# Optimization experiments

Hardware: AMD Instinct MI355X
Metric: run time of the kernel (lower is better)

The kernel has to match this reference:

```python
import jax, jax.numpy as jnp
import numpy as np

N, E, DIN, HID, DOUT = 50000, 800000, 128, 128, 64
NEG_SLOPE = 0.2


def setup_inputs() -> dict:
    key = jax.random.key(0)
    ks = jax.random.split(key, 16)
    x = jax.random.normal(ks[0], (N, DIN), dtype=jnp.float32)
    edge_index = jax.random.randint(ks[1], (2, E), 0, N, dtype=jnp.int64)

    def lin(k, fan_in, fan_out):
        kw, kb = jax.random.split(k)
        s = 1.0 / np.sqrt(fan_in)
        W = jax.random.uniform(kw, (fan_in, fan_out), jnp.float32, -s, s)
        b = jax.random.uniform(kb, (fan_out,), jnp.float32, -s, s)
        return W, b

    Wl, bl = lin(ks[2], DIN, DIN)   # GATv2 lin_l
    Wr, br = lin(ks[3], DIN, DIN)   # GATv2 lin_r
    att = jax.random.uniform(ks[4], (DIN,), jnp.float32, -1.0 / np.sqrt(DIN), 1.0 / np.sqrt(DIN))
    bg = jnp.zeros((DIN,), jnp.float32)  # GAT output bias
    W1, b1 = lin(ks[5], DIN, HID)   # ChebConv K=1 -> plain linear
    W2, b2 = lin(ks[6], HID, HID)
    W3, b3 = lin(ks[7], HID, DOUT)
    return {"x": x, "edge_index": edge_index, "Wl": Wl, "bl": bl, "Wr": Wr,
            "br": br, "att": att, "bg": bg, "W1": W1, "b1": b1,
            "W2": W2, "b2": b2, "W3": W3, "b3": b3}


def reference(x, edge_index, Wl, bl, Wr, br, att, bg, W1, b1, W2, b2, W3, b3):
    n = x.shape[0]
    # GATv2Conv adds self loops by default
    loop = jnp.arange(n, dtype=edge_index.dtype)
    src = jnp.concatenate([edge_index[0], loop])  # source j
    dst = jnp.concatenate([edge_index[1], loop])  # target i

    xl = x @ Wl + bl  # [N, DIN]
    xr = x @ Wr + br  # [N, DIN]

    # GATv2 edge scores: leaky_relu(x_l[j] + x_r[i]) . att
    e = jax.nn.leaky_relu(xl[src] + xr[dst], NEG_SLOPE)  # [E+N, DIN]
    a = e @ att                                          # [E+N]

    # softmax over incoming edges of each destination node
    amax = jax.ops.segment_max(a, dst, num_segments=n)
    ea = jnp.exp(a - amax[dst])
    denom = jax.ops.segment_sum(ea, dst, num_segments=n)
    alpha = ea / denom[dst]                              # [E+N]

    # aggregate messages alpha * x_l[j] at destinations
    h = jax.ops.segment_sum(alpha[:, None] * xl[src], dst, num_segments=n) + bg

    # ChebConv with K=1 reduces to a linear layer (T_0(L) = I)
    h = jax.nn.relu(h @ W1 + b1)
    h = jax.nn.relu(h @ W2 + b2)
    # dropout_rate = 0.0 -> identity
    return h @ W3 + b3
```

## Files before the change

### kernel.cpp

```cpp
#include <hip/hip_runtime.h>
#include <hip/hip_bf16.h>

#define DIN 128
#define NEG_SLOPE 0.2f
#define PTILE 2048
#define FCAP 8192

typedef __attribute__((ext_vector_type(8))) short bf16x8;
typedef __attribute__((ext_vector_type(8))) unsigned short u16x8;
typedef __attribute__((ext_vector_type(4))) float f32x4;

__device__ __forceinline__ ushort f2bf(float f) {
  unsigned u = __float_as_uint(f);
  u += 0x7FFFu + ((u >> 16) & 1u);
  return (ushort)(u >> 16);
}
__device__ __forceinline__ float bf2f(ushort u) {
  return __uint_as_float((unsigned)u << 16);
}

__global__ __launch_bounds__(256) void cvt_weights_kernel(
    const float* __restrict__ Wl, const float* __restrict__ Wr,
    const float* __restrict__ W1, const float* __restrict__ W2,
    const float* __restrict__ W3,
    ushort* __restrict__ WlT, ushort* __restrict__ WrT,
    ushort* __restrict__ W1T, ushort* __restrict__ W2T,
    ushort* __restrict__ W3T, int* __restrict__ ghist) {
  int i = blockIdx.x * 256 + threadIdx.x;
  if (i < 16384) {
    int k = i >> 7, c = i & 127; WlT[c * 128 + k] = f2bf(Wl[i]);
  } else if (i < 32768) {
    int j = i - 16384; int k = j >> 7, c = j & 127; WrT[c * 128 + k] = f2bf(Wr[j]);
  } else if (i < 49152) {
    int j = i - 32768; int k = j >> 7, c = j & 127; W1T[c * 128 + k] = f2bf(W1[j]);
  } else if (i < 65536) {
    int j = i - 49152; int k = j >> 7, c = j & 127; W2T[c * 128 + k] = f2bf(W2[j]);
  } else if (i < 73728) {
    int j = i - 65536; int k = j >> 6, c = j & 63; W3T[c * 128 + k] = f2bf(W3[j]);
  } else if (i < 73984) {
    ghist[i - 73728] = 0;
  }
}

__global__ __launch_bounds__(256) void lin_lr_mfma_kernel(
    const float* __restrict__ x,
    const ushort* __restrict__ WlT, const float* __restrict__ bl,
    const ushort* __restrict__ WrT, const float* __restrict__ br,
    ushort* __restrict__ xl, ushort* __restrict__ xr, int n) {
  const int tid = threadIdx.x;
  const int wv = tid >> 6, lane = tid & 63;
  const int m = lane & 15, quad = lane >> 4;
  const int colbase = (wv & 1) * 64;
  const int nodew = blockIdx.x * 32 + (wv >> 1) * 16;
  int arow = nodew + m; if (arow >= n) arow = n - 1;
  f32x4 accl[4], accr[4];
#pragma unroll
  for (int nt = 0; nt < 4; nt++) { accl[nt] = (f32x4){0,0,0,0}; accr[nt] = (f32x4){0,0,0,0}; }
#pragma unroll
  for (int kk = 0; kk < 4; kk++) {
    int k0 = kk * 32 + quad * 8;
    const float4* xp = (const float4*)(x + (long)arow * 128 + k0);
    float4 x0 = xp[0], x1 = xp[1];
    bf16x8 af;
    af[0] = (short)f2bf(x0.x); af[1] = (short)f2bf(x0.y);
    af[2] = (short)f2bf(x0.z); af[3] = (short)f2bf(x0.w);
    af[4] = (short)f2bf(x1.x); af[5] = (short)f2bf(x1.y);
    af[6] = (short)f2bf(x1.z); af[7] = (short)f2bf(x1.w);
#pragma unroll
    for (int nt = 0; nt < 4; nt++) {
      int brow = colbase + nt * 16 + m;
      bf16x8 bl8 = *(const bf16x8*)(WlT + brow * 128 + k0);
      bf16x8 br8 = *(const bf16x8*)(WrT + brow * 128 + k0);
      accl[nt] = __builtin_amdgcn_mfma_f32_16x16x32_bf16(af, bl8, accl[nt], 0, 0, 0);
      accr[nt] = __builtin_amdgcn_mfma_f32_16x16x32_bf16(af, br8, accr[nt], 0, 0, 0);
    }
  }
#pragma unroll
  for (int nt = 0; nt < 4; nt++) {
    int col = colbase + nt * 16 + m;
    float vbl = bl[col], vbr = br[col];
#pragma unroll
    for (int r = 0; r < 4; r++) {
      int node = nodew + quad * 4 + r;
      if (node < n) {
        xl[(long)node * 128 + col] = f2bf(accl[nt][r] + vbl);
        xr[(long)node * 128 + col] = f2bf(accr[nt][r] + vbr);
      }
    }
  }
}

__global__ __launch_bounds__(256) void hist_kernel(
    const int* __restrict__ ei, int* __restrict__ ghist, int E) {
  __shared__ int h[256];
  h[threadIdx.x] = 0;
  __syncthreads();
  for (int e = blockIdx.x * PTILE + threadIdx.x;
       e < min(E, (int)(blockIdx.x + 1) * PTILE); e += 256)
    atomicAdd(&h[ei[E + e] >> 8], 1);
  __syncthreads();
  if (h[threadIdx.x] > 0) atomicAdd(&ghist[threadIdx.x], h[threadIdx.x]);
}

__global__ __launch_bounds__(256) void scan_small_kernel(
    const int* __restrict__ ghist, int* __restrict__ cum,
    int* __restrict__ cursor) {
  __shared__ int sh[256];
  int tid = threadIdx.x;
  int v = ghist[tid];
  sh[tid] = v;
  __syncthreads();
  for (int d = 1; d < 256; d <<= 1) {
    int t = (tid >= d) ? sh[tid - d] : 0;
    __syncthreads();
    sh[tid] += t;
    __syncthreads();
  }
  int exc = sh[tid] - v;
  cum[tid] = exc;
  cursor[tid] = exc;
  if (tid == 255) cum[256] = sh[255];
}

__global__ __launch_bounds__(256) void partition_kernel(
    const int* __restrict__ ei, unsigned* __restrict__ part,
    int* __restrict__ cursor, int E) {
  __shared__ int hist[256], pref[256], sexcl[256], curs[256], gbase[256];
  __shared__ unsigned buf[PTILE];
  const int tid = threadIdx.x;
  const int tile0 = blockIdx.x * PTILE;
  const int tcount = min(PTILE, E - tile0);
  hist[tid] = 0;
  __syncthreads();
  unsigned pk[PTILE / 256];
  int cnt = 0;
  for (int i = tid; i < tcount; i += 256) {
    int e = tile0 + i;
    int s = ei[e], d = ei[E + e];
    unsigned p = ((unsigned)d << 16) | (unsigned)s;
    pk[cnt++] = p;
    atomicAdd(&hist[d >> 8], 1);
  }
  __syncthreads();
  int v = hist[tid];
  pref[tid] = v;
  __syncthreads();
  for (int d = 1; d < 256; d <<= 1) {
    int t = (tid >= d) ? pref[tid - d] : 0;
    __syncthreads();
    pref[tid] += t;
    __syncthreads();
  }
  int exc = pref[tid] - v;
  sexcl[tid] = exc;
  curs[tid] = exc;
  gbase[tid] = (v > 0) ? atomicAdd(&cursor[tid], v) : 0;
  __syncthreads();
  for (int j = 0; j < cnt; j++) {
    int b = pk[j] >> 24;
    int pos = atomicAdd(&curs[b], 1);
    buf[pos] = pk[j];
  }
  __syncthreads();
  for (int i = tid; i < tcount; i += 256) {
    unsigned p = buf[i];
    int b = p >> 24;
    part[gbase[b] + (i - sexcl[b])] = p;
  }
}

__global__ __launch_bounds__(256) void fine_kernel(
    const unsigned* __restrict__ part, const int* __restrict__ cum,
    int* __restrict__ offsets, int* __restrict__ ssrc,
    int N, int E, int nbuck) {
  __shared__ int hist[256], pref[256], curs[256];
  __shared__ unsigned buf[FCAP], buf2[FCAP];
  const int tid = threadIdx.x;
  const int b = blockIdx.x;
  const int seg0 = cum[b];
  const int len = min(cum[b + 1] - seg0, FCAP);
  hist[tid] = 0;
  __syncthreads();
  for (int i = tid; i < len; i += 256) {
    unsigned p = part[seg0 + i];
    buf[i] = p;
    atomicAdd(&hist[(p >> 16) & 255], 1);
  }
  __syncthreads();
  int v = hist[tid];
  pref[tid] = v;
  __syncthreads();
  for (int d = 1; d < 256; d <<= 1) {
    int t = (tid >= d) ? pref[tid - d] : 0;
    __syncthreads();
    pref[tid] += t;
    __syncthreads();
  }
  int exc = pref[tid] - v;
  curs[tid] = exc;
  int node = b * 256 + tid;
  if (node < N) offsets[node] = seg0 + exc;
  if (b == nbuck - 1 && tid == 0) offsets[N] = E;
  __syncthreads();
  for (int i = tid; i < len; i += 256) {
    unsigned p = buf[i];
    int pos = atomicAdd(&curs[(p >> 16) & 255], 1);
    buf2[pos] = p;
  }
  __syncthreads();
  for (int i = tid; i < len; i += 256)
    ssrc[seg0 + i] = (int)(buf2[i] & 0xFFFFu);
}

__global__ __launch_bounds__(256) void node_aggr_kernel(
    const ushort* __restrict__ xl, const ushort* __restrict__ xr,
    const float* __restrict__ att, const float* __restrict__ bg,
    const int* __restrict__ offsets, const int* __restrict__ ssrc,
    ushort* __restrict__ h, int n) {
  int wave = (int)((blockIdx.x * (long)blockDim.x + threadIdx.x) >> 6);
  int lane = threadIdx.x & 63;
  if (wave >= n) return;
  const int node = wave;
  const int eg = lane >> 4, sl = lane & 15;
  float av[8], r[8], acc[8];
  {
    const float4* ap = (const float4*)(att + sl * 8);
    float4 a0 = ap[0], a1 = ap[1];
    av[0]=a0.x; av[1]=a0.y; av[2]=a0.z; av[3]=a0.w;
    av[4]=a1.x; av[5]=a1.y; av[6]=a1.z; av[7]=a1.w;
  }
  bf16x8 rv = *(const bf16x8*)(xr + (long)node * 128 + sl * 8);
#pragma unroll
  for (int j = 0; j < 8; j++) r[j] = bf2f((ushort)rv[j]);
  bf16x8 lv = *(const bf16x8*)(xl + (long)node * 128 + sl * 8);
  float m;
  {
    float t = 0.f;
#pragma unroll
    for (int j = 0; j < 8; j++) {
      float l = bf2f((ushort)lv[j]);
      acc[j] = (eg == 0) ? l : 0.f;
      float v = l + r[j];
      v = fmaxf(v, 0.f) + NEG_SLOPE * fminf(v, 0.f);
      t += v * av[j];
    }
#pragma unroll
    for (int off = 1; off < 16; off <<= 1) t += __shfl_xor(t, off);
    m = t;
  }
  float denom = (eg == 0) ? 1.f : 0.f;
  const int beg = offsets[node];
  const int end = offsets[node + 1];
  for (int p = beg; p < end; p += 8) {
    int ia = p + eg, ib = p + 4 + eg;
    bool va = ia < end, vb = ib < end;
    int sa = va ? ssrc[ia] : node;
    int sb = vb ? ssrc[ib] : node;
    bf16x8 uva = *(const bf16x8*)(xl + (long)sa * 128 + sl * 8);
    bf16x8 uvb = *(const bf16x8*)(xl + (long)sb * 128 + sl * 8);
    float ua[8], ub[8], ta = 0.f, tb = 0.f;
#pragma unroll
    for (int j = 0; j < 8; j++) {
      ua[j] = bf2f((ushort)uva[j]);
      ub[j] = bf2f((ushort)uvb[j]);
      float wa = ua[j] + r[j]; wa = fmaxf(wa, 0.f) + NEG_SLOPE * fminf(wa, 0.f);
      float wb = ub[j] + r[j]; wb = fmaxf(wb, 0.f) + NEG_SLOPE * fminf(wb, 0.f);
      ta += wa * av[j];
      tb += wb * av[j];
    }
#pragma unroll
    for (int off = 1; off < 16; off <<= 1) {
      ta += __shfl_xor(ta, off);
      tb += __shfl_xor(tb, off);
    }
    ta = va ? ta : -3.0e38f;
    tb = vb ? tb : -3.0e38f;
    float tm = fmaxf(ta, tb);
    tm = fmaxf(tm, __shfl_xor(tm, 16));
    tm = fmaxf(tm, __shfl_xor(tm, 32));
    float mn = fmaxf(m, tm);
    float scale = __expf(m - mn);
    float ea = va ? __expf(ta - mn) : 0.f;
    float eb = vb ? __expf(tb - mn) : 0.f;
    denom = denom * scale + ea + eb;
#pragma unroll
    for (int j = 0; j < 8; j++) acc[j] = acc[j] * scale + ea * ua[j] + eb * ub[j];
    m = mn;
  }
#pragma unroll
  for (int j = 0; j < 8; j++) {
    acc[j] += __shfl_xor(acc[j], 16);
    acc[j] += __shfl_xor(acc[j], 32);
  }
  denom += __shfl_xor(denom, 16);
  denom += __shfl_xor(denom, 32);
  if (eg == 0) {
    float inv = 1.0f / denom;
    const float4* bp = (const float4*)(bg + sl * 8);
    float4 g0 = bp[0], g1 = bp[1];
    float gv[8] = {g0.x, g0.y, g0.z, g0.w, g1.x, g1.y, g1.z, g1.w};
    u16x8 o;
#pragma unroll
    for (int j = 0; j < 8; j++) o[j] = f2bf(acc[j] * inv + gv[j]);
    *(u16x8*)(h + (long)node * 128 + sl * 8) = o;
  }
}

#define LDSP 136
__global__ __launch_bounds__(256) void mlp_mfma_kernel(
    const ushort* __restrict__ hb,
    const ushort* __restrict__ W1T, const float* __restrict__ b1,
    const ushort* __restrict__ W2T, const float* __restrict__ b2,
    const ushort* __restrict__ W3T, const float* __restrict__ b3,
    float* __restrict__ out, int n) {
  __shared__ ushort act[32][LDSP];
  const int tid = threadIdx.x;
  const int wv = tid >> 6, lane = tid & 63;
  const int m = lane & 15, quad = lane >> 4;
  const int half = wv & 1, ng = wv >> 1;
  const int colbase = half * 64;
  const int nodew = blockIdx.x * 32 + ng * 16;
  int arow = nodew + m; if (arow >= n) arow = n - 1;
  f32x4 acc[4];
#pragma unroll
  for (int nt = 0; nt < 4; nt++) acc[nt] = (f32x4){0,0,0,0};
#pragma unroll
  for (int kk = 0; kk < 4; kk++) {
    int k0 = kk * 32 + quad * 8;
    bf16x8 af = *(const bf16x8*)(hb + (long)arow * 128 + k0);
#pragma unroll
    for (int nt = 0; nt < 4; nt++) {
      bf16x8 b8 = *(const bf16x8*)(W1T + (colbase + nt * 16 + m) * 128 + k0);
      acc[nt] = __builtin_amdgcn_mfma_f32_16x16x32_bf16(af, b8, acc[nt], 0, 0, 0);
    }
  }
#pragma unroll
  for (int nt = 0; nt < 4; nt++) {
    int col = colbase + nt * 16 + m;
    float b = b1[col];
#pragma unroll
    for (int r = 0; r < 4; r++)
      act[ng * 16 + quad * 4 + r][col] = f2bf(fmaxf(acc[nt][r] + b, 0.f));
  }
  __syncthreads();
#pragma unroll
  for (int nt = 0; nt < 4; nt++) acc[nt] = (f32x4){0,0,0,0};
#pragma unroll
  for (int kk = 0; kk < 4; kk++) {
    int k0 = kk * 32 + quad * 8;
    bf16x8 af = *(const bf16x8*)(&act[ng * 16 + m][k0]);
#pragma unroll
    for (int nt = 0; nt < 4; nt++) {
      bf16x8 b8 = *(const bf16x8*)(W2T + (colbase + nt * 16 + m) * 128 + k0);
      acc[nt] = __builtin_amdgcn_mfma_f32_16x16x32_bf16(af, b8, acc[nt], 0, 0, 0);
    }
  }
  __syncthreads();
#pragma unroll
  for (int nt = 0; nt < 4; nt++) {
    int col = colbase + nt * 16 + m;
    float b = b2[col];
#pragma unroll
    for (int r = 0; r < 4; r++)
      act[ng * 16 + quad * 4 + r][col] = f2bf(fmaxf(acc[nt][r] + b, 0.f));
  }
  __syncthreads();
  f32x4 acc3[2];
#pragma unroll
  for (int nt = 0; nt < 2; nt++) acc3[nt] = (f32x4){0,0,0,0};
#pragma unroll
  for (int kk = 0; kk < 4; kk++) {
    int k0 = kk * 32 + quad * 8;
    bf16x8 af = *(const bf16x8*)(&act[ng * 16 + m][k0]);
#pragma unroll
    for (int nt = 0; nt < 2; nt++) {
      bf16x8 b8 = *(const bf16x8*)(W3T + (half * 32 + nt * 16 + m) * 128 + k0);
      acc3[nt] = __builtin_amdgcn_mfma_f32_16x16x32_bf16(af, b8, acc3[nt], 0, 0, 0);
    }
  }
#pragma unroll
  for (int nt = 0; nt < 2; nt++) {
    int col = half * 32 + nt * 16 + m;
    float b = b3[col];
#pragma unroll
    for (int r = 0; r < 4; r++) {
      int node = nodew + quad * 4 + r;
      if (node < n) out[(long)node * 64 + col] = acc3[nt][r] + b;
    }
  }
}

extern "C" void kernel_launch(void* const* d_in, const int* in_sizes, int n_in,
                              void* d_out, int out_size, void* d_ws, size_t ws_size,
                              hipStream_t stream) {
  const float* x   = (const float*)d_in[0];
  const int*   ei  = (const int*)d_in[1];
  const float* Wl  = (const float*)d_in[2];
  const float* bl  = (const float*)d_in[3];
  const float* Wr  = (const float*)d_in[4];
  const float* br  = (const float*)d_in[5];
  const float* att = (const float*)d_in[6];
  const float* bg  = (const float*)d_in[7];
  const float* W1  = (const float*)d_in[8];
  const float* b1  = (const float*)d_in[9];
  const float* W2  = (const float*)d_in[10];
  const float* b2  = (const float*)d_in[11];
  const float* W3  = (const float*)d_in[12];
  const float* b3  = (const float*)d_in[13];
  float* out = (float*)d_out;

  const int N = in_sizes[0] / DIN;
  const int E = in_sizes[1] / 2;
  const int nbuck = (N + 255) >> 8;

  char* ws = (char*)d_ws;
  size_t off = 0;
  int* ghist    = (int*)(ws + off);    off += 256 * 4;
  int* cum      = (int*)(ws + off);    off += 257 * 4;
  int* cursor   = (int*)(ws + off);    off += 256 * 4;
  int* offsets  = (int*)(ws + off);    off += ((size_t)N + 4) * 4;
  unsigned* part= (unsigned*)(ws + off); off += (size_t)E * 4;
  int* ssrc     = (int*)(ws + off);    off += (size_t)E * 4;
  ushort* xlb   = (ushort*)(ws + off); off += (size_t)N * DIN * 2;
  ushort* xrb   = (ushort*)(ws + off); off += (size_t)N * DIN * 2;
  ushort* hbf   = (ushort*)(ws + off); off += (size_t)N * DIN * 2;
  ushort* WlT   = (ushort*)(ws + off); off += 16384 * 2;
  ushort* WrT   = (ushort*)(ws + off); off += 16384 * 2;
  ushort* W1T   = (ushort*)(ws + off); off += 16384 * 2;
  ushort* W2T   = (ushort*)(ws + off); off += 16384 * 2;
  ushort* W3T   = (ushort*)(ws + off); off += 8192 * 2;
  (void)ws_size;

  cvt_weights_kernel<<<289, 256, 0, stream>>>(Wl, Wr, W1, W2, W3,
                                              WlT, WrT, W1T, W2T, W3T, ghist);

  int nblk32 = (N + 31) / 32;
  lin_lr_mfma_kernel<<<nblk32, 256, 0, stream>>>(x, WlT, bl, WrT, br,
                                                 xlb, xrb, N);

  int ntile = (E + PTILE - 1) / PTILE;
  hist_kernel<<<ntile, 256, 0, stream>>>(ei, ghist, E);
  scan_small_kernel<<<1, 256, 0, stream>>>(ghist, cum, cursor);
  partition_kernel<<<ntile, 256, 0, stream>>>(ei, part, cursor, E);
  fine_kernel<<<nbuck, 256, 0, stream>>>(part, cum, offsets, ssrc, N, E, nbuck);

  int nwblk = (N + 3) / 4;
  node_aggr_kernel<<<nwblk, 256, 0, stream>>>(xlb, xrb, att, bg,
                                              offsets, ssrc, hbf, N);

  mlp_mfma_kernel<<<nblk32, 256, 0, stream>>>(hbf, W1T, b1, W2T, b2,
                                              W3T, b3, out, N);
}
```

Before: 261.2 us.

## Fuse weight conversion with histogram, widen fine sort, drop online softmax max

The weight conversion and edge histogram now run in one combined launch, with the histogram zeroed by a memset, which removes one kernel launch. The fine bucket-sort kernel uses 512 threads per block so its loads and scatters take fewer passes. Node aggregation drops the running-max online softmax and accumulates exp(score) directly, with fmaf and a cheaper leaky-relu. This removes cross-lane max shuffles and rescaling, but risks overflow if attention scores grow large, since the max subtraction is gone.

```diff
diff --git a/kernel.cpp b/kernel.cpp
--- a/kernel.cpp
+++ b/kernel.cpp
@@ -5,6 +5,7 @@
 #define NEG_SLOPE 0.2f
 #define PTILE 2048
 #define FCAP 8192
+#define CVT_BLKS 289
 
 typedef __attribute__((ext_vector_type(8))) short bf16x8;
 typedef __attribute__((ext_vector_type(8))) unsigned short u16x8;
@@ -19,26 +20,37 @@
   return __uint_as_float((unsigned)u << 16);
 }
 
-__global__ __launch_bounds__(256) void cvt_weights_kernel(
+__global__ __launch_bounds__(256) void cvt_hist_kernel(
     const float* __restrict__ Wl, const float* __restrict__ Wr,
     const float* __restrict__ W1, const float* __restrict__ W2,
     const float* __restrict__ W3,
     ushort* __restrict__ WlT, ushort* __restrict__ WrT,
     ushort* __restrict__ W1T, ushort* __restrict__ W2T,
-    ushort* __restrict__ W3T, int* __restrict__ ghist) {
-  int i = blockIdx.x * 256 + threadIdx.x;
-  if (i < 16384) {
-    int k = i >> 7, c = i & 127; WlT[c * 128 + k] = f2bf(Wl[i]);
-  } else if (i < 32768) {
-    int j = i - 16384; int k = j >> 7, c = j & 127; WrT[c * 128 + k] = f2bf(Wr[j]);
-  } else if (i < 49152) {
-    int j = i - 32768; int k = j >> 7, c = j & 127; W1T[c * 128 + k] = f2bf(W1[j]);
-  } else if (i < 65536) {
-    int j = i - 49152; int k = j >> 7, c = j & 127; W2T[c * 128 + k] = f2bf(W2[j]);
-  } else if (i < 73728) {
-    int j = i - 65536; int k = j >> 6, c = j & 63; W3T[c * 128 + k] = f2bf(W3[j]);
-  } else if (i < 73984) {
-    ghist[i - 73728] = 0;
+    ushort* __restrict__ W3T,
+    const int* __restrict__ ei, int* __restrict__ ghist, int E) {
+  if (blockIdx.x < CVT_BLKS) {
+    int i = blockIdx.x * 256 + threadIdx.x;
+    if (i < 16384) {
+      int k = i >> 7, c = i & 127; WlT[c * 128 + k] = f2bf(Wl[i]);
+    } else if (i < 32768) {
+      int j = i - 16384; int k = j >> 7, c = j & 127; WrT[c * 128 + k] = f2bf(Wr[j]);
+    } else if (i < 49152) {
+      int j = i - 32768; int k = j >> 7, c = j & 127; W1T[c * 128 + k] = f2bf(W1[j]);
+    } else if (i < 65536) {
+      int j = i - 49152; int k = j >> 7, c = j & 127; W2T[c * 128 + k] = f2bf(W2[j]);
+    } else if (i < 73728) {
+      int j = i - 65536; int k = j >> 6, c = j & 63; W3T[c * 128 + k] = f2bf(W3[j]);
+    }
+  } else {
+    __shared__ int h[256];
+    h[threadIdx.x] = 0;
+    __syncthreads();
+    int tile = blockIdx.x - CVT_BLKS;
+    for (int e = tile * PTILE + threadIdx.x;
+         e < min(E, (tile + 1) * PTILE); e += 256)
+      atomicAdd(&h[ei[E + e] >> 8], 1);
+    __syncthreads();
+    if (h[threadIdx.x] > 0) atomicAdd(&ghist[threadIdx.x], h[threadIdx.x]);
   }
 }
 
@@ -90,18 +102,6 @@
   }
 }
 
-__global__ __launch_bounds__(256) void hist_kernel(
-    const int* __restrict__ ei, int* __restrict__ ghist, int E) {
-  __shared__ int h[256];
-  h[threadIdx.x] = 0;
-  __syncthreads();
-  for (int e = blockIdx.x * PTILE + threadIdx.x;
-       e < min(E, (int)(blockIdx.x + 1) * PTILE); e += 256)
-    atomicAdd(&h[ei[E + e] >> 8], 1);
-  __syncthreads();
-  if (h[threadIdx.x] > 0) atomicAdd(&ghist[threadIdx.x], h[threadIdx.x]);
-}
-
 __global__ __launch_bounds__(256) void scan_small_kernel(
     const int* __restrict__ ghist, int* __restrict__ cum,
     int* __restrict__ cursor) {
@@ -169,7 +169,7 @@
   }
 }
 
-__global__ __launch_bounds__(256) void fine_kernel(
+__global__ __launch_bounds__(512) void fine_kernel(
     const unsigned* __restrict__ part, const int* __restrict__ cum,
     int* __restrict__ offsets, int* __restrict__ ssrc,
     int N, int E, int nbuck) {
@@ -179,36 +179,38 @@
   const int b = blockIdx.x;
   const int seg0 = cum[b];
   const int len = min(cum[b + 1] - seg0, FCAP);
-  hist[tid] = 0;
-  __syncthreads();
-  for (int i = tid; i < len; i += 256) {
+  if (tid < 256) hist[tid] = 0;
+  __syncthreads();
+  for (int i = tid; i < len; i += 512) {
     unsigned p = part[seg0 + i];
     buf[i] = p;
     atomicAdd(&hist[(p >> 16) & 255], 1);
   }
   __syncthreads();
-  int v = hist[tid];
-  pref[tid] = v;
+  int v = (tid < 256) ? hist[tid] : 0;
+  if (tid < 256) pref[tid] = v;
   __syncthreads();
   for (int d = 1; d < 256; d <<= 1) {
-    int t = (tid >= d) ? pref[tid - d] : 0;
-    __syncthreads();
-    pref[tid] += t;
-    __syncthreads();
-  }
-  int exc = pref[tid] - v;
-  curs[tid] = exc;
-  int node = b * 256 + tid;
-  if (node < N) offsets[node] = seg0 + exc;
+    int t = (tid >= d && tid < 256) ? pref[tid - d] : 0;
+    __syncthreads();
+    if (tid < 256) pref[tid] += t;
+    __syncthreads();
+  }
+  if (tid < 256) {
+    int exc = pref[tid] - v;
+    curs[tid] = exc;
+    int node = b * 256 + tid;
+    if (node < N) offsets[node] = seg0 + exc;
+  }
   if (b == nbuck - 1 && tid == 0) offsets[N] = E;
   __syncthreads();
-  for (int i = tid; i < len; i += 256) {
+  for (int i = tid; i < len; i += 512) {
     unsigned p = buf[i];
     int pos = atomicAdd(&curs[(p >> 16) & 255], 1);
     buf2[pos] = p;
   }
   __syncthreads();
-  for (int i = tid; i < len; i += 256)
+  for (int i = tid; i < len; i += 512)
     ssrc[seg0 + i] = (int)(buf2[i] & 0xFFFFu);
 }
 
@@ -233,22 +235,24 @@
 #pragma unroll
   for (int j = 0; j < 8; j++) r[j] = bf2f((ushort)rv[j]);
   bf16x8 lv = *(const bf16x8*)(xl + (long)node * 128 + sl * 8);
-  float m;
+  float denom;
   {
     float t = 0.f;
+    float l[8];
 #pragma unroll
     for (int j = 0; j < 8; j++) {
-      float l = bf2f((ushort)lv[j]);
-      acc[j] = (eg == 0) ? l : 0.f;
-      float v = l + r[j];
-      v = fmaxf(v, 0.f) + NEG_SLOPE * fminf(v, 0.f);
-      t += v * av[j];
+      l[j] = bf2f((ushort)lv[j]);
+      float v = l[j] + r[j];
+      v = fmaxf(v, NEG_SLOPE * v);
+      t = fmaf(v, av[j], t);
     }
 #pragma unroll
     for (int off = 1; off < 16; off <<= 1) t += __shfl_xor(t, off);
-    m = t;
-  }
-  float denom = (eg == 0) ? 1.f : 0.f;
+    float es = __expf(t);
+    denom = (eg == 0) ? es : 0.f;
+#pragma unroll
+    for (int j = 0; j < 8; j++) acc[j] = (eg == 0) ? es * l[j] : 0.f;
+  }
   const int beg = offsets[node];
   const int end = offsets[node + 1];
   for (int p = beg; p < end; p += 8) {
@@ -263,29 +267,22 @@
     for (int j = 0; j < 8; j++) {
       ua[j] = bf2f((ushort)uva[j]);
       ub[j] = bf2f((ushort)uvb[j]);
-      float wa = ua[j] + r[j]; wa = fmaxf(wa, 0.f) + NEG_SLOPE * fminf(wa, 0.f);
-      float wb = ub[j] + r[j]; wb = fmaxf(wb, 0.f) + NEG_SLOPE * fminf(wb, 0.f);
-      ta += wa * av[j];
-      tb += wb * av[j];
+      float wa = ua[j] + r[j]; wa = fmaxf(wa, NEG_SLOPE * wa);
+      float wb = ub[j] + r[j]; wb = fmaxf(wb, NEG_SLOPE * wb);
+      ta = fmaf(wa, av[j], ta);
+      tb = fmaf(wb, av[j], tb);
     }
 #pragma unroll
     for (int off = 1; off < 16; off <<= 1) {
       ta += __shfl_xor(ta, off);
       tb += __shfl_xor(tb, off);
     }
-    ta = va ? ta : -3.0e38f;
-    tb = vb ? tb : -3.0e38f;
-    float tm = fmaxf(ta, tb);
-    tm = fmaxf(tm, __shfl_xor(tm, 16));
-    tm = fmaxf(tm, __shfl_xor(tm, 32));
-    float mn = fmaxf(m, tm);
-    float scale = __expf(m - mn);
-    float ea = va ? __expf(ta - mn) : 0.f;
-    float eb = vb ? __expf(tb - mn) : 0.f;
-    denom = denom * scale + ea + eb;
-#pragma unroll
-    for (int j = 0; j < 8; j++) acc[j] = acc[j] * scale + ea * ua[j] + eb * ub[j];
-    m = mn;
+    float ea = va ? __expf(ta) : 0.f;
+    float eb = vb ? __expf(tb) : 0.f;
+    denom += ea + eb;
+#pragma unroll
+    for (int j = 0; j < 8; j++)
+      acc[j] = fmaf(eb, ub[j], fmaf(ea, ua[j], acc[j]));
   }
 #pragma unroll
   for (int j = 0; j < 8; j++) {
@@ -301,7 +298,7 @@
     float gv[8] = {g0.x, g0.y, g0.z, g0.w, g1.x, g1.y, g1.z, g1.w};
     u16x8 o;
 #pragma unroll
-    for (int j = 0; j < 8; j++) o[j] = f2bf(acc[j] * inv + gv[j]);
+    for (int j = 0; j < 8; j++) o[j] = f2bf(fmaf(acc[j], inv, gv[j]));
     *(u16x8*)(h + (long)node * 128 + sl * 8) = o;
   }
 }
@@ -431,18 +428,19 @@
   ushort* W3T   = (ushort*)(ws + off); off += 8192 * 2;
   (void)ws_size;
 
-  cvt_weights_kernel<<<289, 256, 0, stream>>>(Wl, Wr, W1, W2, W3,
-                                              WlT, WrT, W1T, W2T, W3T, ghist);
+  hipMemsetAsync(ghist, 0, 256 * 4, stream);
+
+  int ntile = (E + PTILE - 1) / PTILE;
+  cvt_hist_kernel<<<CVT_BLKS + ntile, 256, 0, stream>>>(
+      Wl, Wr, W1, W2, W3, WlT, WrT, W1T, W2T, W3T, ei, ghist, E);
 
   int nblk32 = (N + 31) / 32;
   lin_lr_mfma_kernel<<<nblk32, 256, 0, stream>>>(x, WlT, bl, WrT, br,
                                                  xlb, xrb, N);
 
-  int ntile = (E + PTILE - 1) / PTILE;
-  hist_kernel<<<ntile, 256, 0, stream>>>(ei, ghist, E);
   scan_small_kernel<<<1, 256, 0, stream>>>(ghist, cum, cursor);
   partition_kernel<<<ntile, 256, 0, stream>>>(ei, part, cursor, E);
-  fine_kernel<<<nbuck, 256, 0, stream>>>(part, cum, offsets, ssrc, N, E, nbuck);
+  fine_kernel<<<nbuck, 512, 0, stream>>>(part, cum, offsets, ssrc, N, E, nbuck);
 
   int nwblk = (N + 3) / 4;
   node_aggr_kernel<<<nwblk, 256, 0, stream>>>(xlb, xrb, att, bg,
```

Measured after the change: 251.7 us. 1.04x faster.
